# Optimization experiments

Hardware: AMD Instinct MI355X
Metric: run time of the kernel (lower is better)

The kernel has to match this reference:

```python
import jax, jax.numpy as jnp
import numpy as np

N = 100000   # n_nodes
E = 800000   # n_edges
IN = 128
HID = 128
OUT = 40
EPS = 1e-5   # BatchNorm1d eps


def setup_inputs() -> dict:
    key = jax.random.key(0)
    ks = jax.random.split(key, 16)
    def w(k, i, o):
        return jax.random.normal(k, (i, o), jnp.float32) / np.sqrt(i).astype(np.float32)
    return {
        "x": jax.random.normal(ks[0], (N, IN), jnp.float32),
        "edge_index": jax.random.randint(ks[1], (2, E), 0, N, dtype=jnp.int64),
        # SAGEConv weights: Wl acts on aggregated neighbors, Wr on root features
        "Wl0": w(ks[2], IN, HID),  "Wr0": w(ks[3], IN, HID),
        "Wl1": w(ks[4], HID, HID), "Wr1": w(ks[5], HID, HID),
        "Wl2": w(ks[6], HID, OUT), "Wr2": w(ks[7], HID, OUT),
        "b2": jnp.zeros((OUT,), jnp.float32),  # bias only on last layer
        # BatchNorm params for layers 0,1 (last layer has no BN)
        "g0": jnp.ones((HID,), jnp.float32), "be0": jnp.zeros((HID,), jnp.float32),
        "g1": jnp.ones((HID,), jnp.float32), "be1": jnp.zeros((HID,), jnp.float32),
    }


def _sage_conv(x, src, dst, Wl, Wr, b=None):
    # mean aggregation of source messages at destination nodes
    msg = x[src]                                             # [E, d] gather
    agg = jax.ops.segment_sum(msg, dst, num_segments=N)      # [N, d]
    cnt = jax.ops.segment_sum(jnp.ones((src.shape[0],), x.dtype), dst,
                              num_segments=N)                # [N]
    mean = agg / jnp.maximum(cnt, 1.0)[:, None]
    out = mean @ Wl + x @ Wr
    if b is not None:
        out = out + b
    return out


def _batch_norm(h, gamma, beta):
    # training-mode BN over node dim, biased variance (matches torch BatchNorm1d)
    mu = h.mean(axis=0)
    var = h.var(axis=0)
    return (h - mu) * jax.lax.rsqrt(var + EPS) * gamma + beta


def reference(x, edge_index, Wl0, Wr0, Wl1, Wr1, Wl2, Wr2, b2, g0, be0, g1, be1):
    src, dst = edge_index[0], edge_index[1]
    h = _sage_conv(x, src, dst, Wl0, Wr0)
    h = jax.nn.relu(_batch_norm(h, g0, be0))
    h = _sage_conv(h, src, dst, Wl1, Wr1)
    h = jax.nn.relu(_batch_norm(h, g1, be1))
    h = _sage_conv(h, src, dst, Wl2, Wr2, b2)
    return h
```

## Files before the change

kernel.cpp:

```cpp
#include <hip/hip_runtime.h>
#include <hip/hip_bf16.h>

#define N_NODES 100000
#define N_EDGES 800000
#define EPS 1e-5f
#define NBANK 32
#define HB_BLOCKS 256
#define HB_PER 3125
#define CS_GPB 64
#define BUCKET_N 12500
#define MROW 68

typedef __attribute__((ext_vector_type(8))) short short8;
typedef __attribute__((ext_vector_type(4))) float floatx4;

__device__ __forceinline__ unsigned short f2b(float f) {
    unsigned int u = __float_as_uint(f);
    u = (u + 0x7fffu + ((u >> 16) & 1u)) >> 16;
    return (unsigned short)u;
}
__device__ __forceinline__ float blo(unsigned int u) { return __uint_as_float(u << 16); }
__device__ __forceinline__ float bhi(unsigned int u) { return __uint_as_float(u & 0xffff0000u); }
__device__ __forceinline__ float b2f(unsigned short s) {
    return __uint_as_float(((unsigned int)s) << 16);
}

__global__ void cvt_f32_bf16(const float* __restrict__ x, unsigned short* __restrict__ o, int n4) {
    int i = blockIdx.x * blockDim.x + threadIdx.x;
    if (i >= n4) return;
    float4 v = ((const float4*)x)[i];
    ushort4 r;
    r.x = f2b(v.x); r.y = f2b(v.y); r.z = f2b(v.z); r.w = f2b(v.w);
    ((ushort4*)o)[i] = r;
}

__global__ void pack_w(const float* __restrict__ Wl, const float* __restrict__ Wr,
                       unsigned short* __restrict__ out, int Hreal, int NCT) {
    int tid = blockIdx.x * blockDim.x + threadIdx.x;
    int total = NCT * 8 * 64 * 8;
    if (tid >= total) return;
    int i = tid & 7;
    int lane = (tid >> 3) & 63;
    int q = tid >> 9;
    int c = q % NCT;
    int t = q / NCT;
    int k = t * 32 + (lane >> 4) * 8 + i;
    int n = c * 16 + (lane & 15);
    float v = 0.f;
    if (n < Hreal) v = (k < 128) ? Wl[k * Hreal + n] : Wr[(k - 128) * Hreal + n];
    out[tid] = f2b(v);
}

__global__ void __launch_bounds__(256) hist_k(const int* __restrict__ dst,
                                              unsigned int* __restrict__ cnt,
                                              unsigned int* __restrict__ bhist) {
    __shared__ unsigned int lh[8];
    if (threadIdx.x < 8) lh[threadIdx.x] = 0;
    __syncthreads();
    int start = blockIdx.x * HB_PER;
    for (int i = threadIdx.x; i < HB_PER; i += 256) {
        int d = dst[start + i];
        atomicAdd(&cnt[d], 1u);
        atomicAdd(&lh[(unsigned int)d / BUCKET_N], 1u);
    }
    __syncthreads();
    if (threadIdx.x < 8) bhist[threadIdx.x * HB_BLOCKS + blockIdx.x] = lh[threadIdx.x];
}

__global__ void bscan(unsigned int* __restrict__ A) {
    __shared__ unsigned int part[256];
    int t = threadIdx.x;
    unsigned int v[8];
    unsigned int s = 0;
#pragma unroll
    for (int i = 0; i < 8; i++) { v[i] = A[t * 8 + i]; s += v[i]; }
    part[t] = s; __syncthreads();
    for (int off = 1; off < 256; off <<= 1) {
        unsigned int add = (t >= off) ? part[t - off] : 0u;
        __syncthreads();
        part[t] += add;
        __syncthreads();
    }
    unsigned int base = part[t] - s;
#pragma unroll
    for (int i = 0; i < 8; i++) { unsigned int old = v[i]; A[t * 8 + i] = base; base += old; }
}

__global__ void __launch_bounds__(256) bscatter(const int* __restrict__ src,
                                                const int* __restrict__ dst,
                                                const unsigned int* __restrict__ boffs,
                                                unsigned int* __restrict__ ebuf) {
    __shared__ unsigned int cur[8];
    if (threadIdx.x < 8) cur[threadIdx.x] = boffs[threadIdx.x * HB_BLOCKS + blockIdx.x];
    __syncthreads();
    int start = blockIdx.x * HB_PER;
    for (int i = threadIdx.x; i < HB_PER; i += 256) {
        int d = dst[start + i];
        int s = src[start + i];
        unsigned int b = (unsigned int)d / BUCKET_N;
        unsigned int dl = (unsigned int)d - b * BUCKET_N;
        unsigned int pos = atomicAdd(&cur[b], 1u);
        ebuf[pos] = (unsigned int)s | (dl << 17);
    }
}

__global__ void __launch_bounds__(256) cscatter(const unsigned int* __restrict__ ebuf,
                                                const unsigned int* __restrict__ rowptr,
                                                unsigned int* __restrict__ cursor,
                                                int* __restrict__ srclist) {
    int g = blockIdx.x & 7;
    int gblk = blockIdx.x >> 3;
    unsigned int estart = rowptr[g * BUCKET_N];
    unsigned int eend = (g == 7) ? N_EDGES : rowptr[(g + 1) * BUCKET_N];
    unsigned int nume = eend - estart;
    unsigned int per = (nume + CS_GPB - 1) / CS_GPB;
    unsigned int s0 = estart + gblk * per;
    unsigned int s1 = s0 + per; if (s1 > eend) s1 = eend;
    unsigned int nodebase = g * BUCKET_N;
    for (unsigned int i = s0 + threadIdx.x; i < s1; i += 256) {
        unsigned int p = ebuf[i];
        unsigned int s = p & 0x1FFFFu;
        unsigned int node = nodebase + (p >> 17);
        unsigned int pos = atomicAdd(&cursor[node], 1u);
        srclist[pos] = (int)s;
    }
}

__global__ void scan1(const unsigned int* __restrict__ cnt, unsigned int* __restrict__ rowptr,
                      unsigned int* __restrict__ bsum) {
    __shared__ unsigned int sh[256];
    int t = threadIdx.x;
    int i = blockIdx.x * 256 + t;
    unsigned int v = (i < N_NODES) ? cnt[i] : 0u;
    sh[t] = v; __syncthreads();
    for (int off = 1; off < 256; off <<= 1) {
        unsigned int add = (t >= off) ? sh[t - off] : 0u;
        __syncthreads();
        sh[t] += add;
        __syncthreads();
    }
    if (i < N_NODES) rowptr[i] = sh[t] - v;
    if (t == 255) bsum[blockIdx.x] = sh[255];
}

__global__ void scan2(const unsigned int* __restrict__ bsum, unsigned int* __restrict__ boff, int nb) {
    __shared__ unsigned int sh[512];
    int t = threadIdx.x;
    unsigned int v = (t < nb) ? bsum[t] : 0u;
    sh[t] = v; __syncthreads();
    for (int off = 1; off < 512; off <<= 1) {
        unsigned int add = (t >= off) ? sh[t - off] : 0u;
        __syncthreads();
        sh[t] += add;
        __syncthreads();
    }
    if (t < nb) boff[t] = sh[t] - v;
}

__global__ void scan3(unsigned int* __restrict__ rowptr, const unsigned int* __restrict__ boff,
                      unsigned int* __restrict__ cursor) {
    int i = blockIdx.x * 256 + threadIdx.x;
    if (i < N_NODES) {
        unsigned int r = rowptr[i] + boff[blockIdx.x];
        rowptr[i] = r;
        cursor[i] = r;
    }
    if (i == N_NODES) rowptr[N_NODES] = N_EDGES;
}

template<int BN>
__device__ __forceinline__ void agg_phase16(const unsigned short* __restrict__ hb,
                                            const unsigned int* __restrict__ rowptr,
                                            const int* __restrict__ srclist,
                                            unsigned int* __restrict__ smean,
                                            const float* __restrict__ sc,
                                            const float* __restrict__ sh,
                                            int wave, int g, int l, int blockrow) {
    const uint4* hp = (const uint4*)hb;
    int nl = wave * 4 + g;
    int node = blockrow + nl;
    float f0 = 0.f, f1 = 0.f, f2 = 0.f, f3 = 0.f, f4 = 0.f, f5 = 0.f, f6 = 0.f, f7 = 0.f;
    float sc0r = 0.f, sc1r = 0.f, sc2r = 0.f, sc3r = 0.f, sc4r = 0.f, sc5r = 0.f, sc6r = 0.f, sc7r = 0.f;
    float sh0r = 0.f, sh1r = 0.f, sh2r = 0.f, sh3r = 0.f, sh4r = 0.f, sh5r = 0.f, sh6r = 0.f, sh7r = 0.f;
    if (BN) {
        const float* s0 = sc + l * 8;
        const float* s1 = sh + l * 8;
        sc0r = s0[0]; sc1r = s0[1]; sc2r = s0[2]; sc3r = s0[3];
        sc4r = s0[4]; sc5r = s0[5]; sc6r = s0[6]; sc7r = s0[7];
        sh0r = s1[0]; sh1r = s1[1]; sh2r = s1[2]; sh3r = s1[3];
        sh4r = s1[4]; sh5r = s1[5]; sh6r = s1[6]; sh7r = s1[7];
    }
    unsigned int b = rowptr[node], e = rowptr[node + 1];
    unsigned int p = b;
#define ACC8(U) { \
    if (BN) { \
        f0 += fmaxf(0.f, fmaf(blo(U.x), sc0r, sh0r)); \
        f1 += fmaxf(0.f, fmaf(bhi(U.x), sc1r, sh1r)); \
        f2 += fmaxf(0.f, fmaf(blo(U.y), sc2r, sh2r)); \
        f3 += fmaxf(0.f, fmaf(bhi(U.y), sc3r, sh3r)); \
        f4 += fmaxf(0.f, fmaf(blo(U.z), sc4r, sh4r)); \
        f5 += fmaxf(0.f, fmaf(bhi(U.z), sc5r, sh5r)); \
        f6 += fmaxf(0.f, fmaf(blo(U.w), sc6r, sh6r)); \
        f7 += fmaxf(0.f, fmaf(bhi(U.w), sc7r, sh7r)); \
    } else { \
        f0 += blo(U.x); f1 += bhi(U.x); f2 += blo(U.y); f3 += bhi(U.y); \
        f4 += blo(U.z); f5 += bhi(U.z); f6 += blo(U.w); f7 += bhi(U.w); \
    } }
    for (; p + 4 <= e; p += 4) {
        int s0 = srclist[p];
        int s1 = srclist[p + 1];
        int s2 = srclist[p + 2];
        int s3 = srclist[p + 3];
        uint4 u0 = hp[(size_t)s0 * 16 + l];
        uint4 u1 = hp[(size_t)s1 * 16 + l];
        uint4 u2 = hp[(size_t)s2 * 16 + l];
        uint4 u3 = hp[(size_t)s3 * 16 + l];
        ACC8(u0); ACC8(u1); ACC8(u2); ACC8(u3);
    }
    if (p + 2 <= e) {
        int s0 = srclist[p];
        int s1 = srclist[p + 1];
        uint4 u0 = hp[(size_t)s0 * 16 + l];
        uint4 u1 = hp[(size_t)s1 * 16 + l];
        ACC8(u0); ACC8(u1);
        p += 2;
    }
    if (p < e) {
        int s0 = srclist[p];
        uint4 u0 = hp[(size_t)s0 * 16 + l];
        ACC8(u0);
    }
#undef ACC8
    unsigned int deg = e - b;
    float r = 1.0f / (float)(deg > 1u ? deg : 1u);
    uint4 o;
    o.x = (unsigned int)f2b(f0 * r) | ((unsigned int)f2b(f1 * r) << 16);
    o.y = (unsigned int)f2b(f2 * r) | ((unsigned int)f2b(f3 * r) << 16);
    o.z = (unsigned int)f2b(f4 * r) | ((unsigned int)f2b(f5 * r) << 16);
    o.w = (unsigned int)f2b(f6 * r) | ((unsigned int)f2b(f7 * r) << 16);
    *(uint4*)&smean[nl * MROW + l * 4] = o;
}

__device__ __forceinline__ short8 bn_pack8(short8 raw, const float* __restrict__ scb,
                                           const float* __restrict__ shb, int koff) {
    short8 r;
#pragma unroll
    for (int i = 0; i < 8; i++) {
        float v = b2f((unsigned short)raw[i]);
        v = fmaxf(0.f, fmaf(v, scb[koff + i], shb[koff + i]));
        r[i] = (short)f2b(v);
    }
    return r;
}

template<int BN>
__global__ void __launch_bounds__(256) gemm2f_k(const unsigned short* __restrict__ hb,
                                                const unsigned int* __restrict__ rowptr,
                                                const int* __restrict__ srclist,
                                                const float* __restrict__ sc,
                                                const float* __restrict__ sh,
                                                const unsigned short* __restrict__ Bp,
                                                unsigned short* __restrict__ outb,
                                                float* __restrict__ sums) {
    __shared__ unsigned int smean[16 * MROW];
    __shared__ float lds_s[128];
    __shared__ float lds_s2[128];
    __shared__ float scb[128];
    __shared__ float shb[128];
    int wave = threadIdx.x >> 6;
    int lane = threadIdx.x & 63;
    int quad = lane >> 4;
    int l15 = lane & 15;
    int blockrow = blockIdx.x * 16;

    if (threadIdx.x < 128) {
        lds_s[threadIdx.x] = 0.f; lds_s2[threadIdx.x] = 0.f;
        if (BN) { scb[threadIdx.x] = sc[threadIdx.x]; shb[threadIdx.x] = sh[threadIdx.x]; }
    }
    if (BN) __syncthreads();

    agg_phase16<BN>(hb, rowptr, srclist, smean, sc, sh, wave, quad, l15, blockrow);
    __syncthreads();

    floatx4 acc[2];
    acc[0] = (floatx4){0.f, 0.f, 0.f, 0.f};
    acc[1] = (floatx4){0.f, 0.f, 0.f, 0.f};

    int r0 = blockrow + l15;

#pragma unroll
    for (int t = 0; t < 8; t++) {
        short8 a0;
        if (t < 4) {
            a0 = *(const short8*)&smean[l15 * MROW + t * 16 + quad * 4];
        } else {
            int koff = (t & 3) * 32 + quad * 8;
            short8 raw = *(const short8*)(hb + (size_t)r0 * 128 + koff);
            a0 = BN ? bn_pack8(raw, scb, shb, koff) : raw;
        }
#pragma unroll
        for (int c = 0; c < 2; c++) {
            int cidx = wave * 2 + c;
            short8 bf = *(const short8*)(Bp + ((size_t)(t * 8 + cidx) * 64 + lane) * 8);
            acc[c] = __builtin_amdgcn_mfma_f32_16x16x32_bf16(a0, bf, acc[c], 0, 0, 0);
        }
    }

#pragma unroll
    for (int c = 0; c < 2; c++) {
        int col = wave * 32 + c * 16 + l15;
        float s = 0.f, s2 = 0.f;
#pragma unroll
        for (int r = 0; r < 4; r++) {
            int row = blockrow + quad * 4 + r;
            float v = acc[c][r];
            outb[(size_t)row * 128 + col] = f2b(v);
            s += v; s2 += v * v;
        }
        s += __shfl_xor(s, 16);  s += __shfl_xor(s, 32);
        s2 += __shfl_xor(s2, 16); s2 += __shfl_xor(s2, 32);
        if (quad == 0) {
            atomicAdd(&lds_s[col], s);
            atomicAdd(&lds_s2[col], s2);
        }
    }

    __syncthreads();
    if (threadIdx.x < 128) {
        int bank = blockIdx.x & (NBANK - 1);
        atomicAdd(&sums[bank * 256 + threadIdx.x], lds_s[threadIdx.x]);
        atomicAdd(&sums[bank * 256 + 128 + threadIdx.x], lds_s2[threadIdx.x]);
    }
}

__global__ void __launch_bounds__(256) dense_k(const unsigned short* __restrict__ hb,
                                               const float* __restrict__ sc,
                                               const float* __restrict__ sh,
                                               const unsigned short* __restrict__ Bp,
                                               const float* __restrict__ bias,
                                               unsigned short* __restrict__ P,
                                               float* __restrict__ Q) {
    __shared__ float scb[128];
    __shared__ float shb[128];
    int wave = threadIdx.x >> 6;
    int lane = threadIdx.x & 63;
    int quad = lane >> 4;
    int l15 = lane & 15;
    int blockrow = blockIdx.x * 16;

    if (threadIdx.x < 128) { scb[threadIdx.x] = sc[threadIdx.x]; shb[threadIdx.x] = sh[threadIdx.x]; }
    __syncthreads();

    int r0 = blockrow + l15;
    short8 af[4];
#pragma unroll
    for (int t = 0; t < 4; t++) {
        int koff = t * 32 + quad * 8;
        short8 raw = *(const short8*)(hb + (size_t)r0 * 128 + koff);
        af[t] = bn_pack8(raw, scb, shb, koff);
    }

    if (wave < 3) {
        floatx4 aP = (floatx4){0.f, 0.f, 0.f, 0.f};
        floatx4 aQ = (floatx4){0.f, 0.f, 0.f, 0.f};
#pragma unroll
        for (int t = 0; t < 4; t++) {
            short8 bl = *(const short8*)(Bp + ((size_t)(t * 3 + wave) * 64 + lane) * 8);
            aP = __builtin_amdgcn_mfma_f32_16x16x32_bf16(af[t], bl, aP, 0, 0, 0);
        }
#pragma unroll
        for (int t = 0; t < 4; t++) {
            short8 br = *(const short8*)(Bp + ((size_t)((t + 4) * 3 + wave) * 64 + lane) * 8);
            aQ = __builtin_amdgcn_mfma_f32_16x16x32_bf16(af[t], br, aQ, 0, 0, 0);
        }
        int col = wave * 16 + l15;
#pragma unroll
        for (int r = 0; r < 4; r++) {
            int row = blockrow + quad * 4 + r;
            P[(size_t)row * 64 + col] = f2b(aP[r]);
        }
        if (col < 40) {
#pragma unroll
            for (int r = 0; r < 4; r++) {
                int row = blockrow + quad * 4 + r;
                Q[(size_t)row * 40 + col] = aQ[r] + bias[col];
            }
        }
    } else {
#pragma unroll
        for (int r = 0; r < 4; r++) {
            int row = blockrow + quad * 4 + r;
            P[(size_t)row * 64 + 48 + l15] = 0;
        }
    }
}

__global__ void __launch_bounds__(256) agg40_k(const unsigned short* __restrict__ P,
                                               const unsigned int* __restrict__ rowptr,
                                               const int* __restrict__ srclist,
                                               const float* __restrict__ Q,
                                               float* __restrict__ out) {
    int tid = threadIdx.x;
    int g = tid >> 3;
    int l = tid & 7;
    int node = blockIdx.x * 32 + g;
    const uint4* pp = (const uint4*)P;
    float f0 = 0.f, f1 = 0.f, f2 = 0.f, f3 = 0.f, f4 = 0.f, f5 = 0.f, f6 = 0.f, f7 = 0.f;
    unsigned int b = rowptr[node], e = rowptr[node + 1];
    unsigned int p = b;
#define ACC8(U) { f0 += blo(U.x); f1 += bhi(U.x); f2 += blo(U.y); f3 += bhi(U.y); \
                  f4 += blo(U.z); f5 += bhi(U.z); f6 += blo(U.w); f7 += bhi(U.w); }
    for (; p + 4 <= e; p += 4) {
        int s0 = srclist[p];
        int s1 = srclist[p + 1];
        int s2 = srclist[p + 2];
        int s3 = srclist[p + 3];
        uint4 u0 = pp[(size_t)s0 * 8 + l];
        uint4 u1 = pp[(size_t)s1 * 8 + l];
        uint4 u2 = pp[(size_t)s2 * 8 + l];
        uint4 u3 = pp[(size_t)s3 * 8 + l];
        ACC8(u0); ACC8(u1); ACC8(u2); ACC8(u3);
    }
    if (p + 2 <= e) {
        int s0 = srclist[p];
        int s1 = srclist[p + 1];
        uint4 u0 = pp[(size_t)s0 * 8 + l];
        uint4 u1 = pp[(size_t)s1 * 8 + l];
        ACC8(u0); ACC8(u1);
        p += 2;
    }
    if (p < e) {
        int s0 = srclist[p];
        uint4 u0 = pp[(size_t)s0 * 8 + l];
        ACC8(u0);
    }
#undef ACC8
    unsigned int deg = e - b;
    float r = 1.0f / (float)(deg > 1u ? deg : 1u);
    if (l < 5) {
        size_t base = (size_t)node * 40 + l * 8;
        float4 o1, o2;
        o1.x = f0 * r + Q[base + 0]; o1.y = f1 * r + Q[base + 1];
        o1.z = f2 * r + Q[base + 2]; o1.w = f3 * r + Q[base + 3];
        o2.x = f4 * r + Q[base + 4]; o2.y = f5 * r + Q[base + 5];
        o2.z = f6 * r + Q[base + 6]; o2.w = f7 * r + Q[base + 7];
        *(float4*)(out + base) = o1;
        *(float4*)(out + base + 4) = o2;
    }
}

__global__ void bn_finalize(const float* __restrict__ sums, const float* __restrict__ g,
                            const float* __restrict__ be, float* __restrict__ sc,
                            float* __restrict__ sh) {
    __shared__ float lds[256];
    int t = threadIdx.x;
    float s = 0.f;
#pragma unroll 8
    for (int bk = 0; bk < NBANK; bk++) s += sums[bk * 256 + t];
    lds[t] = s;
    __syncthreads();
    if (t < 128) {
        float inv_n = 1.0f / (float)N_NODES;
        float mu = lds[t] * inv_n;
        float var = lds[128 + t] * inv_n - mu * mu;
        float sf = g[t] * rsqrtf(var + EPS);
        sc[t] = sf;
        sh[t] = be[t] - mu * sf;
    }
}

extern "C" void kernel_launch(void* const* d_in, const int* in_sizes, int n_in,
                              void* d_out, int out_size, void* d_ws, size_t ws_size,
                              hipStream_t stream) {
    const float* x   = (const float*)d_in[0];
    const int* ei    = (const int*)d_in[1];
    const float* Wl0 = (const float*)d_in[2];
    const float* Wr0 = (const float*)d_in[3];
    const float* Wl1 = (const float*)d_in[4];
    const float* Wr1 = (const float*)d_in[5];
    const float* Wl2 = (const float*)d_in[6];
    const float* Wr2 = (const float*)d_in[7];
    const float* b2  = (const float*)d_in[8];
    const float* g0  = (const float*)d_in[9];
    const float* be0 = (const float*)d_in[10];
    const float* g1  = (const float*)d_in[11];
    const float* be1 = (const float*)d_in[12];

    char* ws = (char*)d_ws;
    size_t off = 0;
    auto alloc = [&](size_t bytes) -> void* {
        void* p = ws + off;
        off += (bytes + 4095) & ~(size_t)4095;
        return p;
    };

    const size_t NB16 = (size_t)N_NODES * 128 * 2;
    unsigned short* xb   = (unsigned short*)alloc(NB16);
    unsigned short* C0b  = (unsigned short*)alloc(NB16);
    unsigned short* C1b  = (unsigned short*)alloc(NB16);
    unsigned int* cnt    = (unsigned int*)alloc((size_t)N_NODES * 4);
    unsigned int* rowptr = (unsigned int*)alloc((size_t)(N_NODES + 1) * 4);
    unsigned int* cursor = (unsigned int*)alloc((size_t)N_NODES * 4);
    int* srclist         = (int*)alloc((size_t)N_EDGES * 4);
    unsigned int* ebuf   = (unsigned int*)alloc((size_t)N_EDGES * 4);
    unsigned int* bhist  = (unsigned int*)alloc(8 * HB_BLOCKS * 4);
    unsigned int* bsum   = (unsigned int*)alloc(512 * 4);
    unsigned int* boff   = (unsigned int*)alloc(512 * 4);
    float* sums0         = (float*)alloc(NBANK * 256 * 4);
    float* sums1         = (float*)alloc(NBANK * 256 * 4);
    float* sc            = (float*)alloc(128 * 4);
    float* sh            = (float*)alloc(128 * 4);
    unsigned short* W0p  = (unsigned short*)alloc(8 * 8 * 64 * 8 * 2);
    unsigned short* W1p  = (unsigned short*)alloc(8 * 8 * 64 * 8 * 2);
    unsigned short* W2p  = (unsigned short*)alloc(3 * 8 * 64 * 8 * 2);

    unsigned short* P64  = C0b;
    float* Q             = (float*)xb;

    const int* srcp = ei;
    const int* dstp = ei + N_EDGES;

    hipMemsetAsync(cnt, 0, (size_t)N_NODES * 4, stream);
    hipMemsetAsync(sums0, 0, (size_t)2 * NBANK * 256 * 4, stream);
    cvt_f32_bf16<<<12500, 256, 0, stream>>>(x, xb, N_NODES * 32);
    pack_w<<<(8 * 4096 + 255) / 256, 256, 0, stream>>>(Wl0, Wr0, W0p, 128, 8);
    pack_w<<<(8 * 4096 + 255) / 256, 256, 0, stream>>>(Wl1, Wr1, W1p, 128, 8);
    pack_w<<<(3 * 4096 + 255) / 256, 256, 0, stream>>>(Wl2, Wr2, W2p, 40, 3);

    hist_k<<<HB_BLOCKS, 256, 0, stream>>>(dstp, cnt, bhist);
    scan1<<<391, 256, 0, stream>>>(cnt, rowptr, bsum);
    scan2<<<1, 512, 0, stream>>>(bsum, boff, 391);
    scan3<<<391, 256, 0, stream>>>(rowptr, boff, cursor);
    bscan<<<1, 256, 0, stream>>>(bhist);
    bscatter<<<HB_BLOCKS, 256, 0, stream>>>(srcp, dstp, bhist, ebuf);
    cscatter<<<8 * CS_GPB, 256, 0, stream>>>(ebuf, rowptr, cursor, srclist);

    gemm2f_k<0><<<6250, 256, 0, stream>>>(xb, rowptr, srclist, nullptr, nullptr, W0p, C0b, sums0);
    bn_finalize<<<1, 256, 0, stream>>>(sums0, g0, be0, sc, sh);

    gemm2f_k<1><<<6250, 256, 0, stream>>>(C0b, rowptr, srclist, sc, sh, W1p, C1b, sums1);
    bn_finalize<<<1, 256, 0, stream>>>(sums1, g1, be1, sc, sh);

    dense_k<<<6250, 256, 0, stream>>>(C1b, sc, sh, W2p, b2, P64, Q);
    agg40_k<<<3125, 256, 0, stream>>>(P64, rowptr, srclist, Q, (float*)d_out);

    (void)in_sizes; (void)n_in; (void)out_size; (void)ws_size;
}
```

Baseline: 360.6 us.

## Merge preprocessing kernels, prefetch edge indices, compact final-layer P rows to 40

Merges the conversion and histogram kernels, the three weight-pack kernels, and the scan and scatter stages into fewer launches, and folds two memsets into one contiguous memset. The gather loops in both aggregation kernels now load the next group of source indices before accumulating the current rows, which overlaps index loads with feature loads. The last-layer projection P shrinks from 64 to 40 bf16 columns per row, so the gather reads less, and dense_k drops its padding wave and runs with 192 threads. In exchange, merged kernels carry heterogeneous blocks, and lanes 5-7 in agg40 read duplicate addresses.

```diff
diff --git a/kernel.cpp b/kernel.cpp
--- a/kernel.cpp
+++ b/kernel.cpp
@@ -25,20 +25,37 @@
     return __uint_as_float(((unsigned int)s) << 16);
 }
 
-__global__ void cvt_f32_bf16(const float* __restrict__ x, unsigned short* __restrict__ o, int n4) {
-    int i = blockIdx.x * blockDim.x + threadIdx.x;
-    if (i >= n4) return;
-    float4 v = ((const float4*)x)[i];
-    ushort4 r;
-    r.x = f2b(v.x); r.y = f2b(v.y); r.z = f2b(v.z); r.w = f2b(v.w);
-    ((ushort4*)o)[i] = r;
-}
-
-__global__ void pack_w(const float* __restrict__ Wl, const float* __restrict__ Wr,
-                       unsigned short* __restrict__ out, int Hreal, int NCT) {
-    int tid = blockIdx.x * blockDim.x + threadIdx.x;
-    int total = NCT * 8 * 64 * 8;
-    if (tid >= total) return;
+__global__ void __launch_bounds__(256) prep_k(const float* __restrict__ x,
+                                              unsigned short* __restrict__ o,
+                                              const int* __restrict__ dst,
+                                              unsigned int* __restrict__ cnt,
+                                              unsigned int* __restrict__ bhist) {
+    if (blockIdx.x < 12500) {
+        int i = blockIdx.x * 256 + threadIdx.x;
+        float4 v = ((const float4*)x)[i];
+        ushort4 r;
+        r.x = f2b(v.x); r.y = f2b(v.y); r.z = f2b(v.z); r.w = f2b(v.w);
+        ((ushort4*)o)[i] = r;
+        return;
+    }
+    __shared__ unsigned int lh[8];
+    int hb = blockIdx.x - 12500;
+    if (threadIdx.x < 8) lh[threadIdx.x] = 0;
+    __syncthreads();
+    int start = hb * HB_PER;
+    for (int i = threadIdx.x; i < HB_PER; i += 256) {
+        int d = dst[start + i];
+        atomicAdd(&cnt[d], 1u);
+        atomicAdd(&lh[(unsigned int)d / BUCKET_N], 1u);
+    }
+    __syncthreads();
+    if (threadIdx.x < 8) bhist[threadIdx.x * HB_BLOCKS + hb] = lh[threadIdx.x];
+}
+
+__device__ __forceinline__ void pack_one(const float* __restrict__ Wl,
+                                         const float* __restrict__ Wr,
+                                         unsigned short* __restrict__ out,
+                                         int Hreal, int NCT, int tid) {
     int i = tid & 7;
     int lane = (tid >> 3) & 63;
     int q = tid >> 9;
@@ -51,49 +68,96 @@
     out[tid] = f2b(v);
 }
 
-__global__ void __launch_bounds__(256) hist_k(const int* __restrict__ dst,
-                                              unsigned int* __restrict__ cnt,
-                                              unsigned int* __restrict__ bhist) {
-    __shared__ unsigned int lh[8];
-    if (threadIdx.x < 8) lh[threadIdx.x] = 0;
-    __syncthreads();
-    int start = blockIdx.x * HB_PER;
-    for (int i = threadIdx.x; i < HB_PER; i += 256) {
-        int d = dst[start + i];
-        atomicAdd(&cnt[d], 1u);
-        atomicAdd(&lh[(unsigned int)d / BUCKET_N], 1u);
-    }
-    __syncthreads();
-    if (threadIdx.x < 8) bhist[threadIdx.x * HB_BLOCKS + blockIdx.x] = lh[threadIdx.x];
-}
-
-__global__ void bscan(unsigned int* __restrict__ A) {
+__global__ void __launch_bounds__(256) pack_all(const float* __restrict__ Wl0, const float* __restrict__ Wr0,
+                                                const float* __restrict__ Wl1, const float* __restrict__ Wr1,
+                                                const float* __restrict__ Wl2, const float* __restrict__ Wr2,
+                                                unsigned short* __restrict__ W0p,
+                                                unsigned short* __restrict__ W1p,
+                                                unsigned short* __restrict__ W2p) {
+    int tid = blockIdx.x * 256 + threadIdx.x;
+    if (tid < 32768) pack_one(Wl0, Wr0, W0p, 128, 8, tid);
+    else if (tid < 65536) pack_one(Wl1, Wr1, W1p, 128, 8, tid - 32768);
+    else if (tid < 77824) pack_one(Wl2, Wr2, W2p, 40, 3, tid - 65536);
+}
+
+__global__ void scan1(const unsigned int* __restrict__ cnt, unsigned int* __restrict__ rowptr,
+                      unsigned int* __restrict__ bsum) {
+    __shared__ unsigned int sh[256];
+    int t = threadIdx.x;
+    int i = blockIdx.x * 256 + t;
+    unsigned int v = (i < N_NODES) ? cnt[i] : 0u;
+    sh[t] = v; __syncthreads();
+    for (int off = 1; off < 256; off <<= 1) {
+        unsigned int add = (t >= off) ? sh[t - off] : 0u;
+        __syncthreads();
+        sh[t] += add;
+        __syncthreads();
+    }
+    if (i < N_NODES) rowptr[i] = sh[t] - v;
+    if (t == 255) bsum[blockIdx.x] = sh[255];
+}
+
+__global__ void scan2_bscan(const unsigned int* __restrict__ bsum, unsigned int* __restrict__ boff,
+                            int nb, unsigned int* __restrict__ A) {
+    if (blockIdx.x == 0) {
+        __shared__ unsigned int sh[512];
+        int t = threadIdx.x;
+        unsigned int v = (t < nb) ? bsum[t] : 0u;
+        sh[t] = v; __syncthreads();
+        for (int off = 1; off < 512; off <<= 1) {
+            unsigned int add = (t >= off) ? sh[t - off] : 0u;
+            __syncthreads();
+            sh[t] += add;
+            __syncthreads();
+        }
+        if (t < nb) boff[t] = sh[t] - v;
+        return;
+    }
     __shared__ unsigned int part[256];
     int t = threadIdx.x;
     unsigned int v[8];
     unsigned int s = 0;
-#pragma unroll
-    for (int i = 0; i < 8; i++) { v[i] = A[t * 8 + i]; s += v[i]; }
-    part[t] = s; __syncthreads();
+    if (t < 256) {
+#pragma unroll
+        for (int i = 0; i < 8; i++) { v[i] = A[t * 8 + i]; s += v[i]; }
+        part[t] = s;
+    }
+    __syncthreads();
     for (int off = 1; off < 256; off <<= 1) {
-        unsigned int add = (t >= off) ? part[t - off] : 0u;
+        unsigned int add = (t < 256 && t >= off) ? part[t - off] : 0u;
         __syncthreads();
-        part[t] += add;
+        if (t < 256) part[t] += add;
         __syncthreads();
     }
-    unsigned int base = part[t] - s;
-#pragma unroll
-    for (int i = 0; i < 8; i++) { unsigned int old = v[i]; A[t * 8 + i] = base; base += old; }
-}
-
-__global__ void __launch_bounds__(256) bscatter(const int* __restrict__ src,
-                                                const int* __restrict__ dst,
-                                                const unsigned int* __restrict__ boffs,
-                                                unsigned int* __restrict__ ebuf) {
+    if (t < 256) {
+        unsigned int base = part[t] - s;
+#pragma unroll
+        for (int i = 0; i < 8; i++) { unsigned int old = v[i]; A[t * 8 + i] = base; base += old; }
+    }
+}
+
+__global__ void __launch_bounds__(256) scan3_bscatter(unsigned int* __restrict__ rowptr,
+                                                      const unsigned int* __restrict__ boff,
+                                                      unsigned int* __restrict__ cursor,
+                                                      const int* __restrict__ src,
+                                                      const int* __restrict__ dst,
+                                                      const unsigned int* __restrict__ boffs,
+                                                      unsigned int* __restrict__ ebuf) {
+    if (blockIdx.x < 391) {
+        int i = blockIdx.x * 256 + threadIdx.x;
+        if (i < N_NODES) {
+            unsigned int r = rowptr[i] + boff[blockIdx.x];
+            rowptr[i] = r;
+            cursor[i] = r;
+        }
+        if (i == N_NODES) rowptr[N_NODES] = N_EDGES;
+        return;
+    }
     __shared__ unsigned int cur[8];
-    if (threadIdx.x < 8) cur[threadIdx.x] = boffs[threadIdx.x * HB_BLOCKS + blockIdx.x];
-    __syncthreads();
-    int start = blockIdx.x * HB_PER;
+    int bb = blockIdx.x - 391;
+    if (threadIdx.x < 8) cur[threadIdx.x] = boffs[threadIdx.x * HB_BLOCKS + bb];
+    __syncthreads();
+    int start = bb * HB_PER;
     for (int i = threadIdx.x; i < HB_PER; i += 256) {
         int d = dst[start + i];
         int s = src[start + i];
@@ -124,48 +188,6 @@
         unsigned int pos = atomicAdd(&cursor[node], 1u);
         srclist[pos] = (int)s;
     }
-}
-
-__global__ void scan1(const unsigned int* __restrict__ cnt, unsigned int* __restrict__ rowptr,
-                      unsigned int* __restrict__ bsum) {
-    __shared__ unsigned int sh[256];
-    int t = threadIdx.x;
-    int i = blockIdx.x * 256 + t;
-    unsigned int v = (i < N_NODES) ? cnt[i] : 0u;
-    sh[t] = v; __syncthreads();
-    for (int off = 1; off < 256; off <<= 1) {
-        unsigned int add = (t >= off) ? sh[t - off] : 0u;
-        __syncthreads();
-        sh[t] += add;
-        __syncthreads();
-    }
-    if (i < N_NODES) rowptr[i] = sh[t] - v;
-    if (t == 255) bsum[blockIdx.x] = sh[255];
-}
-
-__global__ void scan2(const unsigned int* __restrict__ bsum, unsigned int* __restrict__ boff, int nb) {
-    __shared__ unsigned int sh[512];
-    int t = threadIdx.x;
-    unsigned int v = (t < nb) ? bsum[t] : 0u;
-    sh[t] = v; __syncthreads();
-    for (int off = 1; off < 512; off <<= 1) {
-        unsigned int add = (t >= off) ? sh[t - off] : 0u;
-        __syncthreads();
-        sh[t] += add;
-        __syncthreads();
-    }
-    if (t < nb) boff[t] = sh[t] - v;
-}
-
-__global__ void scan3(unsigned int* __restrict__ rowptr, const unsigned int* __restrict__ boff,
-                      unsigned int* __restrict__ cursor) {
-    int i = blockIdx.x * 256 + threadIdx.x;
-    if (i < N_NODES) {
-        unsigned int r = rowptr[i] + boff[blockIdx.x];
-        rowptr[i] = r;
-        cursor[i] = r;
-    }
-    if (i == N_NODES) rowptr[N_NODES] = N_EDGES;
 }
 
 template<int BN>
@@ -206,28 +228,30 @@
         f0 += blo(U.x); f1 += bhi(U.x); f2 += blo(U.y); f3 += bhi(U.y); \
         f4 += blo(U.z); f5 += bhi(U.z); f6 += blo(U.w); f7 += bhi(U.w); \
     } }
-    for (; p + 4 <= e; p += 4) {
-        int s0 = srclist[p];
-        int s1 = srclist[p + 1];
-        int s2 = srclist[p + 2];
-        int s3 = srclist[p + 3];
+    int s0 = 0, s1 = 0, s2 = 0, s3 = 0;
+    bool have = (p + 4 <= e);
+    if (have) { s0 = srclist[p]; s1 = srclist[p + 1]; s2 = srclist[p + 2]; s3 = srclist[p + 3]; }
+    while (have) {
         uint4 u0 = hp[(size_t)s0 * 16 + l];
         uint4 u1 = hp[(size_t)s1 * 16 + l];
         uint4 u2 = hp[(size_t)s2 * 16 + l];
         uint4 u3 = hp[(size_t)s3 * 16 + l];
+        p += 4;
+        have = (p + 4 <= e);
+        if (have) { s0 = srclist[p]; s1 = srclist[p + 1]; s2 = srclist[p + 2]; s3 = srclist[p + 3]; }
         ACC8(u0); ACC8(u1); ACC8(u2); ACC8(u3);
     }
     if (p + 2 <= e) {
-        int s0 = srclist[p];
-        int s1 = srclist[p + 1];
-        uint4 u0 = hp[(size_t)s0 * 16 + l];
-        uint4 u1 = hp[(size_t)s1 * 16 + l];
+        int t0 = srclist[p];
+        int t1 = srclist[p + 1];
+        uint4 u0 = hp[(size_t)t0 * 16 + l];
+        uint4 u1 = hp[(size_t)t1 * 16 + l];
         ACC8(u0); ACC8(u1);
         p += 2;
     }
     if (p < e) {
-        int s0 = srclist[p];
-        uint4 u0 = hp[(size_t)s0 * 16 + l];
+        int t0 = srclist[p];
+        uint4 u0 = hp[(size_t)t0 * 16 + l];
         ACC8(u0);
     }
 #undef ACC8
@@ -333,7 +357,7 @@
     }
 }
 
-__global__ void __launch_bounds__(256) dense_k(const unsigned short* __restrict__ hb,
+__global__ void __launch_bounds__(192) dense_k(const unsigned short* __restrict__ hb,
                                                const float* __restrict__ sc,
                                                const float* __restrict__ sh,
                                                const unsigned short* __restrict__ Bp,
@@ -360,37 +384,25 @@
         af[t] = bn_pack8(raw, scb, shb, koff);
     }
 
-    if (wave < 3) {
-        floatx4 aP = (floatx4){0.f, 0.f, 0.f, 0.f};
-        floatx4 aQ = (floatx4){0.f, 0.f, 0.f, 0.f};
-#pragma unroll
-        for (int t = 0; t < 4; t++) {
-            short8 bl = *(const short8*)(Bp + ((size_t)(t * 3 + wave) * 64 + lane) * 8);
-            aP = __builtin_amdgcn_mfma_f32_16x16x32_bf16(af[t], bl, aP, 0, 0, 0);
-        }
-#pragma unroll
-        for (int t = 0; t < 4; t++) {
-            short8 br = *(const short8*)(Bp + ((size_t)((t + 4) * 3 + wave) * 64 + lane) * 8);
-            aQ = __builtin_amdgcn_mfma_f32_16x16x32_bf16(af[t], br, aQ, 0, 0, 0);
-        }
-        int col = wave * 16 + l15;
+    floatx4 aP = (floatx4){0.f, 0.f, 0.f, 0.f};
+    floatx4 aQ = (floatx4){0.f, 0.f, 0.f, 0.f};
+#pragma unroll
+    for (int t = 0; t < 4; t++) {
+        short8 bl = *(const short8*)(Bp + ((size_t)(t * 3 + wave) * 64 + lane) * 8);
+        aP = __builtin_amdgcn_mfma_f32_16x16x32_bf16(af[t], bl, aP, 0, 0, 0);
+    }
+#pragma unroll
+    for (int t = 0; t < 4; t++) {
+        short8 br = *(const short8*)(Bp + ((size_t)((t + 4) * 3 + wave) * 64 + lane) * 8);
+        aQ = __builtin_amdgcn_mfma_f32_16x16x32_bf16(af[t], br, aQ, 0, 0, 0);
+    }
+    int col = wave * 16 + l15;
+    if (col < 40) {
 #pragma unroll
         for (int r = 0; r < 4; r++) {
             int row = blockrow + quad * 4 + r;
-            P[(size_t)row * 64 + col] = f2b(aP[r]);
-        }
-        if (col < 40) {
-#pragma unroll
-            for (int r = 0; r < 4; r++) {
-                int row = blockrow + quad * 4 + r;
-                Q[(size_t)row * 40 + col] = aQ[r] + bias[col];
-            }
-        }
-    } else {
-#pragma unroll
-        for (int r = 0; r < 4; r++) {
-            int row = blockrow + quad * 4 + r;
-            P[(size_t)row * 64 + 48 + l15] = 0;
+            P[(size_t)row * 40 + col] = f2b(aP[r]);
+            Q[(size_t)row * 40 + col] = aQ[r] + bias[col];
         }
     }
 }
@@ -403,6 +415,7 @@
     int tid = threadIdx.x;
     int g = tid >> 3;
     int l = tid & 7;
+    int ll = l < 5 ? l : 0;
     int node = blockIdx.x * 32 + g;
     const uint4* pp = (const uint4*)P;
     float f0 = 0.f, f1 = 0.f, f2 = 0.f, f3 = 0.f, f4 = 0.f, f5 = 0.f, f6 = 0.f, f7 = 0.f;
@@ -410,28 +423,30 @@
     unsigned int p = b;
 #define ACC8(U) { f0 += blo(U.x); f1 += bhi(U.x); f2 += blo(U.y); f3 += bhi(U.y); \
                   f4 += blo(U.z); f5 += bhi(U.z); f6 += blo(U.w); f7 += bhi(U.w); }
-    for (; p + 4 <= e; p += 4) {
-        int s0 = srclist[p];
-        int s1 = srclist[p + 1];
-        int s2 = srclist[p + 2];
-        int s3 = srclist[p + 3];
-        uint4 u0 = pp[(size_t)s0 * 8 + l];
-        uint4 u1 = pp[(size_t)s1 * 8 + l];
-        uint4 u2 = pp[(size_t)s2 * 8 + l];
-        uint4 u3 = pp[(size_t)s3 * 8 + l];
+    int s0 = 0, s1 = 0, s2 = 0, s3 = 0;
+    bool have = (p + 4 <= e);
+    if (have) { s0 = srclist[p]; s1 = srclist[p + 1]; s2 = srclist[p + 2]; s3 = srclist[p + 3]; }
+    while (have) {
+        uint4 u0 = pp[(size_t)s0 * 5 + ll];
+        uint4 u1 = pp[(size_t)s1 * 5 + ll];
+        uint4 u2 = pp[(size_t)s2 * 5 + ll];
+        uint4 u3 = pp[(size_t)s3 * 5 + ll];
+        p += 4;
+        have = (p + 4 <= e);
+        if (have) { s0 = srclist[p]; s1 = srclist[p + 1]; s2 = srclist[p + 2]; s3 = srclist[p + 3]; }
         ACC8(u0); ACC8(u1); ACC8(u2); ACC8(u3);
     }
     if (p + 2 <= e) {
-        int s0 = srclist[p];
-        int s1 = srclist[p + 1];
-        uint4 u0 = pp[(size_t)s0 * 8 + l];
-        uint4 u1 = pp[(size_t)s1 * 8 + l];
+        int t0 = srclist[p];
+        int t1 = srclist[p + 1];
+        uint4 u0 = pp[(size_t)t0 * 5 + ll];
+        uint4 u1 = pp[(size_t)t1 * 5 + ll];
         ACC8(u0); ACC8(u1);
         p += 2;
     }
     if (p < e) {
-        int s0 = srclist[p];
-        uint4 u0 = pp[(size_t)s0 * 8 + l];
+        int t0 = srclist[p];
+        uint4 u0 = pp[(size_t)t0 * 5 + ll];
         ACC8(u0);
     }
 #undef ACC8
@@ -499,6 +514,8 @@
     unsigned short* C0b  = (unsigned short*)alloc(NB16);
     unsigned short* C1b  = (unsigned short*)alloc(NB16);
     unsigned int* cnt    = (unsigned int*)alloc((size_t)N_NODES * 4);
+    float* sums0         = (float*)alloc(NBANK * 256 * 4);
+    float* sums1         = (float*)alloc(NBANK * 256 * 4);
     unsigned int* rowptr = (unsigned int*)alloc((size_t)(N_NODES + 1) * 4);
     unsigned int* cursor = (unsigned int*)alloc((size_t)N_NODES * 4);
     int* srclist         = (int*)alloc((size_t)N_EDGES * 4);
@@ -506,33 +523,28 @@
     unsigned int* bhist  = (unsigned int*)alloc(8 * HB_BLOCKS * 4);
     unsigned int* bsum   = (unsigned int*)alloc(512 * 4);
     unsigned int* boff   = (unsigned int*)alloc(512 * 4);
-    float* sums0         = (float*)alloc(NBANK * 256 * 4);
-    float* sums1         = (float*)alloc(NBANK * 256 * 4);
     float* sc            = (float*)alloc(128 * 4);
     float* sh            = (float*)alloc(128 * 4);
     unsigned short* W0p  = (unsigned short*)alloc(8 * 8 * 64 * 8 * 2);
     unsigned short* W1p  = (unsigned short*)alloc(8 * 8 * 64 * 8 * 2);
     unsigned short* W2p  = (unsigned short*)alloc(3 * 8 * 64 * 8 * 2);
 
-    unsigned short* P64  = C0b;
+    unsigned short* P40  = C0b;
     float* Q             = (float*)xb;
 
     const int* srcp = ei;
     const int* dstp = ei + N_EDGES;
 
-    hipMemsetAsync(cnt, 0, (size_t)N_NODES * 4, stream);
-    hipMemsetAsync(sums0, 0, (size_t)2 * NBANK * 256 * 4, stream);
-    cvt_f32_bf16<<<12500, 256, 0, stream>>>(x, xb, N_NODES * 32);
-    pack_w<<<(8 * 4096 + 255) / 256, 256, 0, stream>>>(Wl0, Wr0, W0p, 128, 8);
-    pack_w<<<(8 * 4096 + 255) / 256, 256, 0, stream>>>(Wl1, Wr1, W1p, 128, 8);
-    pack_w<<<(3 * 4096 + 255) / 256, 256, 0, stream>>>(Wl2, Wr2, W2p, 40, 3);
-
-    hist_k<<<HB_BLOCKS, 256, 0, stream>>>(dstp, cnt, bhist);
+    size_t cnt_slab  = ((size_t)N_NODES * 4 + 4095) & ~(size_t)4095;
+    size_t sums_slab = ((size_t)NBANK * 256 * 4 + 4095) & ~(size_t)4095;
+    hipMemsetAsync(cnt, 0, cnt_slab + 2 * sums_slab, stream);
+
+    prep_k<<<12756, 256, 0, stream>>>(x, xb, dstp, cnt, bhist);
+    pack_all<<<304, 256, 0, stream>>>(Wl0, Wr0, Wl1, Wr1, Wl2, Wr2, W0p, W1p, W2p);
+
     scan1<<<391, 256, 0, stream>>>(cnt, rowptr, bsum);
-    scan2<<<1, 512, 0, stream>>>(bsum, boff, 391);
-    scan3<<<391, 256, 0, stream>>>(rowptr, boff, cursor);
-    bscan<<<1, 256, 0, stream>>>(bhist);
-    bscatter<<<HB_BLOCKS, 256, 0, stream>>>(srcp, dstp, bhist, ebuf);
+    scan2_bscan<<<2, 512, 0, stream>>>(bsum, boff, 391, bhist);
+    scan3_bscatter<<<647, 256, 0, stream>>>(rowptr, boff, cursor, srcp, dstp, bhist, ebuf);
     cscatter<<<8 * CS_GPB, 256, 0, stream>>>(ebuf, rowptr, cursor, srclist);
 
     gemm2f_k<0><<<6250, 256, 0, stream>>>(xb, rowptr, srclist, nullptr, nullptr, W0p, C0b, sums0);
@@ -541,8 +553,8 @@
     gemm2f_k<1><<<6250, 256, 0, stream>>>(C0b, rowptr, srclist, sc, sh, W1p, C1b, sums1);
     bn_finalize<<<1, 256, 0, stream>>>(sums1, g1, be1, sc, sh);
 
-    dense_k<<<6250, 256, 0, stream>>>(C1b, sc, sh, W2p, b2, P64, Q);
-    agg40_k<<<3125, 256, 0, stream>>>(P64, rowptr, srclist, Q, (float*)d_out);
+    dense_k<<<6250, 192, 0, stream>>>(C1b, sc, sh, W2p, b2, P40, Q);
+    agg40_k<<<3125, 256, 0, stream>>>(P40, rowptr, srclist, Q, (float*)d_out);
 
     (void)in_sizes; (void)n_in; (void)out_size; (void)ws_size;
 }
```

Result: no change. 360.2 us (-0.1%).
